# Optimization experiments

Hardware: AMD Instinct MI355X
Metric: run time of the kernel (lower is better)

Reference implementation:

```python
import jax, jax.numpy as jnp
import numpy as np

GROUPS = 32
EPS = 1e-5
NUM_HEADS = 8
HEAD_DIM = 64
CHANNELS = 512


def group_norm(x, scale, bias):
    # x: [b, h, w, c]; normalize over (h, w, channels-within-group)
    b, h, w, c = x.shape
    xg = x.reshape(b, h, w, GROUPS, c // GROUPS)
    mean = jnp.mean(xg, axis=(1, 2, 4), keepdims=True)
    var = jnp.var(xg, axis=(1, 2, 4), keepdims=True)
    xg = (xg - mean) * jax.lax.rsqrt(var + EPS)
    return xg.reshape(b, h, w, c) * scale + bias


def setup_inputs() -> dict:
    key = jax.random.key(0)
    ks = jax.random.split(key, 8)
    b, hs, ws, c = 8, 32, 32, CHANNELS
    inner = NUM_HEADS * HEAD_DIM
    return {
        "x": jax.random.normal(ks[0], (b, hs, ws, c), dtype=jnp.float32),
        "t": jax.random.normal(ks[1], (b,), dtype=jnp.float32),
        "gn_scale": jnp.ones((c,), dtype=jnp.float32),
        "gn_bias": jnp.zeros((c,), dtype=jnp.float32),
        "w_qkv": jax.random.normal(ks[2], (c, 3 * inner), dtype=jnp.float32) * 0.02,
        "b_qkv": jnp.zeros((3 * inner,), dtype=jnp.float32),
        "w_out": jax.random.normal(ks[3], (inner, c), dtype=jnp.float32) * 0.02,
        "b_out": jnp.zeros((c,), dtype=jnp.float32),
    }


def reference(x, t, gn_scale, gn_bias, w_qkv, b_qkv, w_out, b_out):
    b, hs, ws, c = x.shape
    # NOTE: original reassigns x = GroupNorm(x); the residual uses the NORMALIZED x.
    xn = group_norm(x, gn_scale, gn_bias)
    x_flat = xn.reshape(b, hs * ws, c)                      # [b, s, c]
    qkv = x_flat @ w_qkv + b_qkv                            # [b, s, 3*nh*hd]
    qkv = qkv.reshape(b, hs * ws, NUM_HEADS, 3 * HEAD_DIM)
    q, k, v = jnp.split(qkv, 3, axis=-1)                    # each [b, s, nh, hd]
    q = q / jnp.sqrt(jnp.float32(HEAD_DIM))
    q = q.transpose(0, 2, 1, 3)                             # [b, nh, s, hd]
    k = k.transpose(0, 2, 1, 3)
    v = v.transpose(0, 2, 1, 3)
    attn = jax.nn.softmax(jnp.einsum('bhqd,bhkd->bhqk', q, k), axis=-1)
    out = jnp.einsum('bhqk,bhkd->bhqd', attn, v)            # [b, nh, s, hd]
    out = out.transpose(0, 2, 1, 3).reshape(b, hs * ws, NUM_HEADS * HEAD_DIM)
    h = out @ w_out + b_out                                 # [b, s, c]
    h = h.reshape(b, hs, ws, c)
    return xn + h
```

## Files before the change

### kernel.cpp

```cpp
#include <hip/hip_runtime.h>
#include <hip/hip_bf16.h>


#define B_    8
#define S_    1024
#define C_    512
#define NH    8
#define HD    64
#define QKVC  1536
#define GROUPS 32
#define GSIZE  16
#define EPSV   1e-5f
#define QSCL  0.18033688f

using frag8 = __attribute__((ext_vector_type(8))) short;
using f32x4 = __attribute__((ext_vector_type(4))) float;

__device__ __forceinline__ float bf2f(unsigned short u) {
    union { unsigned int i; float f; } v; v.i = ((unsigned int)u) << 16; return v.f;
}
__device__ __forceinline__ unsigned short f2bf(float f) {
    union { float f; unsigned int i; } v; v.f = f;
    unsigned int x = v.i;
    return (unsigned short)((x + 0x7fffu + ((x >> 16) & 1u)) >> 16);
}
__device__ __forceinline__ unsigned int pk2bf(float a, float b) {
    union { float f; unsigned int u; } x, y; x.f = a; y.f = b;
    return __builtin_amdgcn_perm(y.u + 0x8000u, x.u + 0x8000u, 0x07060302u);
}
__device__ __forceinline__ float fexp2(float x) {
#if __has_builtin(__builtin_amdgcn_exp2f)
    return __builtin_amdgcn_exp2f(x);
#else
    return exp2f(x);
#endif
}
__device__ __forceinline__ f32x4 zero4() {
    f32x4 z; z[0] = 0.f; z[1] = 0.f; z[2] = 0.f; z[3] = 0.f; return z;
}
__device__ __forceinline__ void gl_lds(const unsigned short* gp, unsigned short* lp) {
    __builtin_amdgcn_global_load_lds(
        (const __attribute__((address_space(1))) void*)gp,
        (__attribute__((address_space(3))) void*)lp, 16, 0, 0);
}

__global__ __launch_bounds__(256) void prep_kernel(
        const float* __restrict__ w_qkv, const float* __restrict__ w_out,
        unsigned short* __restrict__ wqkvT, unsigned short* __restrict__ woutT,
        const float* __restrict__ x,
        const float* __restrict__ scale, const float* __restrict__ bias,
        unsigned short* __restrict__ xn) {
    __shared__ unsigned short xcache[16384];
    __shared__ float s_red[8];
    int id = blockIdx.x;
    int t = threadIdx.x;
    if (id < 1024) {
        float* tile = (float*)xcache;
        const float* in; unsigned short* out; int N, n0, k0;
        if (id < 768) { in = w_qkv; out = wqkvT; N = QKVC; n0 = (id % 48) * 32; k0 = (id / 48) * 32; }
        else { int i2 = id - 768; in = w_out; out = woutT; N = C_; n0 = (i2 % 16) * 32; k0 = (i2 / 16) * 32; }
        for (int i = 0; i < 4; ++i) {
            int idx = t + i * 256; int r = idx >> 5, c = idx & 31;
            tile[r * 33 + c] = in[(size_t)(k0 + r) * N + n0 + c];
        }
        __syncthreads();
        for (int i = 0; i < 4; ++i) {
            int idx = t + i * 256; int r = idx >> 5, c = idx & 31;
            out[(size_t)(n0 + r) * C_ + k0 + c] = f2bf(tile[c * 33 + r]);
        }
        return;
    }
    int bg = id - 1024;
    int b = bg >> 5, g = bg & 31;
    const float* xb = x + (size_t)b * S_ * C_;

    float sum = 0.f, ss = 0.f;
    for (int i = 0; i < 16; ++i) {
        int idx = t + i * 256;
        int row = idx >> 2, j = idx & 3;
        float4 v = *(const float4*)(xb + (size_t)row * C_ + g * GSIZE + j * 4);
        sum += v.x + v.y + v.z + v.w;
        ss  += v.x * v.x + v.y * v.y + v.z * v.z + v.w * v.w;
        uint2 c;
        c.x = pk2bf(v.x, v.y);
        c.y = pk2bf(v.z, v.w);
        *(uint2*)(&xcache[idx * 4]) = c;
    }
    for (int off = 1; off < 64; off <<= 1) {
        sum += __shfl_xor(sum, off);
        ss  += __shfl_xor(ss,  off);
    }
    int wid = t >> 6;
    if ((t & 63) == 0) { s_red[wid] = sum; s_red[4 + wid] = ss; }
    __syncthreads();
    sum = s_red[0] + s_red[1] + s_red[2] + s_red[3];
    ss  = s_red[4] + s_red[5] + s_red[6] + s_red[7];
    float mean = sum * (1.f / 16384.f);
    float var  = ss * (1.f / 16384.f) - mean * mean;
    float rinv = rsqrtf(var + EPSV);

    float sc[16], bi[16];
    for (int u = 0; u < 16; ++u) {
        sc[u] = scale[g * GSIZE + u];
        bi[u] = bias[g * GSIZE + u];
    }
    for (int i = 0; i < 16; ++i) {
        int idx = t + i * 256;
        int row = idx >> 2, j = idx & 3;
        uint2 c = *(const uint2*)(&xcache[idx * 4]);
        float v0 = bf2f((unsigned short)(c.x & 0xffffu));
        float v1 = bf2f((unsigned short)(c.x >> 16));
        float v2 = bf2f((unsigned short)(c.y & 0xffffu));
        float v3 = bf2f((unsigned short)(c.y >> 16));
        int c0 = j * 4;
        float f0 = (v0 - mean) * rinv * sc[c0 + 0] + bi[c0 + 0];
        float f1 = (v1 - mean) * rinv * sc[c0 + 1] + bi[c0 + 1];
        float f2 = (v2 - mean) * rinv * sc[c0 + 2] + bi[c0 + 2];
        float f3 = (v3 - mean) * rinv * sc[c0 + 3] + bi[c0 + 3];
        uint2 o;
        o.x = pk2bf(f0, f1);
        o.y = pk2bf(f2, f3);
        *(uint2*)(xn + (size_t)b * S_ * C_ + (size_t)row * C_ + g * GSIZE + c0) = o;
    }
}

__global__ __launch_bounds__(256) void gemm_qkv_kernel(
        const unsigned short* __restrict__ A,
        const unsigned short* __restrict__ Bt,
        const float* __restrict__ bias,
        unsigned short* __restrict__ outA,
        unsigned short* __restrict__ outV) {
    __shared__ unsigned short As[2][128 * 32];
    __shared__ unsigned short Bs[2][128 * 32];
    unsigned int flat = blockIdx.y * 12u + blockIdx.x;
    unsigned int nid = (flat & 7u) * 96u + (flat >> 3);
    int my = nid / 12u, mx = nid % 12u;
    int m0 = my * 128, n0 = mx * 128;
    int t = threadIdx.x;
    int wid = t >> 6, lane = t & 63;
    int quad = lane >> 4, l16 = lane & 15;
    int wm = (wid >> 1) * 64, wn = (wid & 1) * 64;

    f32x4 acc[4][4];
    for (int mi = 0; mi < 4; ++mi)
        for (int ni = 0; ni < 4; ++ni) acc[mi][ni] = zero4();

    int srow = t >> 2, sseg = t & 3;
    auto stage = [&](int k0, int buf) {
        for (int i = 0; i < 2; ++i) {
            gl_lds(A + (size_t)(m0 + i * 64 + srow) * C_ + k0 + sseg * 8,
                   &As[buf][(size_t)(i * 256 + wid * 64) * 8]);
            gl_lds(Bt + (size_t)(n0 + i * 64 + srow) * C_ + k0 + sseg * 8,
                   &Bs[buf][(size_t)(i * 256 + wid * 64) * 8]);
        }
    };

    stage(0, 0);
    const int nk = C_ >> 5;
    for (int i = 0; i < nk; ++i) {
        __syncthreads();
        if (i + 1 < nk) stage((i + 1) << 5, (i + 1) & 1);
        int buf = i & 1;

        frag8 bfrag[4], afrag[4];
        for (int ni = 0; ni < 4; ++ni)
            bfrag[ni] = *(const frag8*)(&Bs[buf][(wn + ni * 16 + l16) * 32 + quad * 8]);
        for (int mi = 0; mi < 4; ++mi)
            afrag[mi] = *(const frag8*)(&As[buf][(wm + mi * 16 + l16) * 32 + quad * 8]);

        for (int mi = 0; mi < 4; ++mi)
            for (int ni = 0; ni < 4; ++ni)
                acc[mi][ni] = __builtin_amdgcn_mfma_f32_16x16x32_bf16(
                    afrag[mi], bfrag[ni], acc[mi][ni], 0, 0, 0);
    }

    for (int ni = 0; ni < 4; ++ni) {
        int c0 = n0 + wn + ni * 16;
        float bv = bias[c0 + l16];
        int h = c0 / 192, rr = c0 % 192;
        if (rr >= 128) {
            int d = rr - 128 + l16;
            int bidx = m0 >> 10;
            unsigned short* vp = outV + (((size_t)bidx * NH + h) * HD + d) * S_
                               + (m0 & 1023) + wm + quad * 4;
            for (int mi = 0; mi < 4; ++mi) {
                uint2 pk;
                pk.x = pk2bf(acc[mi][ni][0] + bv, acc[mi][ni][1] + bv);
                pk.y = pk2bf(acc[mi][ni][2] + bv, acc[mi][ni][3] + bv);
                *(uint2*)(vp + mi * 16) = pk;
            }
        } else {
            float scl = (rr < 64) ? QSCL : 1.0f;
            int colk = h * 128 + rr + l16;
            for (int mi = 0; mi < 4; ++mi)
                for (int r = 0; r < 4; ++r) {
                    int row = m0 + wm + mi * 16 + quad * 4 + r;
                    outA[(size_t)row * 1024 + colk] = f2bf((acc[mi][ni][r] + bv) * scl);
                }
        }
    }
}

__global__ __launch_bounds__(256) void gemm_out_kernel(
        const unsigned short* __restrict__ A,
        const unsigned short* __restrict__ Bt,
        const float* __restrict__ bias,
        const unsigned short* __restrict__ resid,
        float* __restrict__ outF) {
    __shared__ unsigned short As[2][64 * 32];
    __shared__ unsigned short Bs[2][128 * 32];
    unsigned int flat = blockIdx.x;
    unsigned int nid = (flat & 7u) * 64u + (flat >> 3);
    int my = nid >> 2, mx = nid & 3;
    int m0 = my * 64, n0 = mx * 128;
    int t = threadIdx.x;
    int wid = t >> 6, lane = t & 63;
    int quad = lane >> 4, l16 = lane & 15;
    int wm = (wid >> 1) * 32, wn = (wid & 1) * 64;

    f32x4 acc[2][4];
    for (int mi = 0; mi < 2; ++mi)
        for (int ni = 0; ni < 4; ++ni) acc[mi][ni] = zero4();

    int srow = t >> 2, sseg = t & 3;
    auto stage = [&](int k0, int buf) {
        gl_lds(A + (size_t)(m0 + srow) * C_ + k0 + sseg * 8,
               &As[buf][(size_t)wid * 512]);
        for (int i = 0; i < 2; ++i)
            gl_lds(Bt + (size_t)(n0 + i * 64 + srow) * C_ + k0 + sseg * 8,
                   &Bs[buf][(size_t)(i * 256 + wid * 64) * 8]);
    };

    stage(0, 0);
    const int nk = C_ >> 5;
    for (int i = 0; i < nk; ++i) {
        __syncthreads();
        if (i + 1 < nk) stage((i + 1) << 5, (i + 1) & 1);
        int buf = i & 1;

        frag8 bfrag[4], afrag[2];
        for (int ni = 0; ni < 4; ++ni)
            bfrag[ni] = *(const frag8*)(&Bs[buf][(wn + ni * 16 + l16) * 32 + quad * 8]);
        for (int mi = 0; mi < 2; ++mi)
            afrag[mi] = *(const frag8*)(&As[buf][(wm + mi * 16 + l16) * 32 + quad * 8]);

        for (int mi = 0; mi < 2; ++mi)
            for (int ni = 0; ni < 4; ++ni)
                acc[mi][ni] = __builtin_amdgcn_mfma_f32_16x16x32_bf16(
                    afrag[mi], bfrag[ni], acc[mi][ni], 0, 0, 0);
    }

    for (int ni = 0; ni < 4; ++ni) {
        int col = n0 + wn + ni * 16 + l16;
        float bv = bias[col];
        for (int mi = 0; mi < 2; ++mi)
            for (int r = 0; r < 4; ++r) {
                int row = m0 + wm + mi * 16 + quad * 4 + r;
                float v = acc[mi][ni][r] + bv + bf2f(resid[(size_t)row * C_ + col]);
                outF[(size_t)row * C_ + col] = v;
            }
    }
}

__global__ __launch_bounds__(256) void attn_kernel(
        const unsigned short* __restrict__ kq,
        const unsigned short* __restrict__ vT,
        unsigned short* __restrict__ attn_out) {
    int i = blockIdx.x;
    int xcd = i & 7, slot = i >> 3;
    int bh = xcd * 8 + (slot >> 3);
    int qt = slot & 7;
    int b = bh >> 3, h = bh & 7;

    int t = threadIdx.x;
    int wid = t >> 6, lane = t & 63, quad = lane >> 4, l16 = lane & 15;
    int q0 = qt * 128 + wid * 32;

    __shared__ unsigned short Ks[2][2][2048];
    __shared__ unsigned short Vs[2][2][2048];

    const unsigned short* qrow0 = kq + ((size_t)b * S_ + q0 + l16) * 1024 + h * 128;
    const unsigned short* qrow1 = qrow0 + (size_t)16 * 1024;
    frag8 qf[2][2];
    qf[0][0] = *(const frag8*)(qrow0 + quad * 8);
    qf[0][1] = *(const frag8*)(qrow0 + 32 + quad * 8);
    qf[1][0] = *(const frag8*)(qrow1 + quad * 8);
    qf[1][1] = *(const frag8*)(qrow1 + 32 + quad * 8);

    frag8 ones;
    for (int i2 = 0; i2 < 8; ++i2) ones[i2] = (short)0x3f80;

    f32x4 o[2][4], ol[2];
    for (int g = 0; g < 2; ++g) {
        ol[g] = zero4();
        for (int dt = 0; dt < 4; ++dt) o[g][dt] = zero4();
    }

    const unsigned short* kbase = kq + (size_t)b * S_ * 1024 + h * 128 + 64;
    const unsigned short* vbase = vT + ((size_t)b * NH + h) * HD * S_;

    int kdh = wid & 1, krh = wid >> 1;
    int krow = krh * 16 + (lane >> 2);
    int kseg = (lane & 3) ^ ((lane >> 3) & 3);
    int vd = wid * 16 + (lane >> 2);
    int vseg = lane & 3;
    int vkh = vseg >> 1, vsp = vseg & 1;
    int vsw = (lane >> 3) & 3;
    int vo1 = (((vsp * 2) ^ vsw) * 8) + vkh * 4;
    int vo2 = (((vsp * 2 + 1) ^ vsw) * 8) + vkh * 4;

    int ksw = (l16 >> 1) & 3;

    auto stageK = [&](int j0, int buf, int half) {
        gl_lds(kbase + (size_t)(j0 + krow) * 1024 + kdh * 32 + kseg * 8,
               &Ks[buf][half][kdh * 1024 + krh * 512]);
    };
    auto loadV = [&](int j0) {
        return *(const uint4*)(vbase + (size_t)vd * S_ + j0 + vseg * 8);
    };
    auto writeV = [&](uint4 w, int buf, int half) {
        unsigned short* vdst = &Vs[buf][half][vd * 32];
        uint2 g1; g1.x = w.x; g1.y = w.y;
        uint2 g2; g2.x = w.z; g2.y = w.w;
        *(uint2*)(vdst + vo1) = g1;
        *(uint2*)(vdst + vo2) = g2;
    };

    stageK(0, 0, 0);  stageK(32, 0, 1);
    writeV(loadV(0), 0, 0);  writeV(loadV(32), 0, 1);

    for (int it = 0; it < S_ / 64; ++it) {
        int cur = it & 1, nxt = cur ^ 1;
        __syncthreads();
        uint4 vn0, vn1;
        bool more = (it < S_ / 64 - 1);
        if (more) {
            int jn = (it + 1) * 64;
            stageK(jn, nxt, 0);
            stageK(jn + 32, nxt, 1);
            vn0 = loadV(jn);
            vn1 = loadV(jn + 32);
        }

        for (int half = 0; half < 2; ++half) {
            frag8 kf[2][2];
            for (int kh = 0; kh < 2; ++kh)
                for (int dh = 0; dh < 2; ++dh)
                    kf[kh][dh] = *(const frag8*)(&Ks[cur][half][dh * 1024
                        + (kh * 16 + l16) * 32 + ((quad ^ ksw) * 8)]);

            frag8 vf[4];
            for (int dt = 0; dt < 4; ++dt)
                vf[dt] = *(const frag8*)(&Vs[cur][half][(dt * 16 + l16) * 32
                        + ((quad ^ ksw) * 8)]);

            for (int g = 0; g < 2; ++g) {
                f32x4 s0 = zero4(), s1 = zero4();
                __builtin_amdgcn_s_setprio(1);
                s0 = __builtin_amdgcn_mfma_f32_16x16x32_bf16(kf[0][0], qf[g][0], s0, 0, 0, 0);
                s0 = __builtin_amdgcn_mfma_f32_16x16x32_bf16(kf[0][1], qf[g][1], s0, 0, 0, 0);
                s1 = __builtin_amdgcn_mfma_f32_16x16x32_bf16(kf[1][0], qf[g][0], s1, 0, 0, 0);
                s1 = __builtin_amdgcn_mfma_f32_16x16x32_bf16(kf[1][1], qf[g][1], s1, 0, 0, 0);
                __builtin_amdgcn_s_setprio(0);

                union { frag8 f; unsigned int u[4]; } pfu;
                pfu.u[0] = pk2bf(fexp2(s0[0]), fexp2(s0[1]));
                pfu.u[1] = pk2bf(fexp2(s0[2]), fexp2(s0[3]));
                pfu.u[2] = pk2bf(fexp2(s1[0]), fexp2(s1[1]));
                pfu.u[3] = pk2bf(fexp2(s1[2]), fexp2(s1[3]));

                __builtin_amdgcn_s_setprio(1);
                ol[g] = __builtin_amdgcn_mfma_f32_16x16x32_bf16(pfu.f, ones, ol[g], 0, 0, 0);
                for (int dt = 0; dt < 4; ++dt)
                    o[g][dt] = __builtin_amdgcn_mfma_f32_16x16x32_bf16(pfu.f, vf[dt], o[g][dt], 0, 0, 0);
                __builtin_amdgcn_s_setprio(0);
            }
        }

        if (more) {
            writeV(vn0, nxt, 0);
            writeV(vn1, nxt, 1);
        }
    }

    for (int g = 0; g < 2; ++g)
        for (int r = 0; r < 4; ++r) {
            float inv = 1.0f / ol[g][r];
            int qrw = q0 + g * 16 + quad * 4 + r;
            for (int dt = 0; dt < 4; ++dt) {
                int ch = h * HD + dt * 16 + l16;
                attn_out[((size_t)b * S_ + qrw) * C_ + ch] = f2bf(o[g][dt][r] * inv);
            }
        }
}

extern "C" void kernel_launch(void* const* d_in, const int* in_sizes, int n_in,
                              void* d_out, int out_size, void* d_ws, size_t ws_size,
                              hipStream_t stream) {
    const float* x        = (const float*)d_in[0];
    const float* gn_scale = (const float*)d_in[2];
    const float* gn_bias  = (const float*)d_in[3];
    const float* w_qkv    = (const float*)d_in[4];
    const float* b_qkv    = (const float*)d_in[5];
    const float* w_out    = (const float*)d_in[6];
    const float* b_out    = (const float*)d_in[7];
    float* out = (float*)d_out;

    char* ws = (char*)d_ws;
    unsigned short* xn    = (unsigned short*)(ws);
    unsigned short* kq    = (unsigned short*)(ws + ((size_t)8  << 20));
    unsigned short* attn  = (unsigned short*)(ws + ((size_t)24 << 20));
    unsigned short* vT    = (unsigned short*)(ws + ((size_t)32 << 20));
    unsigned short* wqkvT = (unsigned short*)(ws + ((size_t)40 << 20));
    unsigned short* woutT = (unsigned short*)(ws + ((size_t)40 << 20) + ((size_t)3 << 19));

    prep_kernel<<<dim3(1280), 256, 0, stream>>>(
        w_qkv, w_out, wqkvT, woutT, x, gn_scale, gn_bias, xn);

    gemm_qkv_kernel<<<dim3(QKVC / 128, (B_ * S_) / 128), 256, 0, stream>>>(
        xn, wqkvT, b_qkv, kq, vT);

    attn_kernel<<<dim3(512), 256, 0, stream>>>(kq, vT, attn);

    gemm_out_kernel<<<dim3(512), 256, 0, stream>>>(
        attn, woutT, b_out, xn, out);
}
```

Measured before the change: 152.3 us.

## Swizzle LDS tiles in GEMMs, remap groupnorm blocks per XCD, pack transpose stores

Result: no change. 149.9 us (-1.5%).

```diff
diff --git a/kernel.cpp b/kernel.cpp
--- a/kernel.cpp
+++ b/kernel.cpp
@@ -64,14 +64,18 @@
             tile[r * 33 + c] = in[(size_t)(k0 + r) * N + n0 + c];
         }
         __syncthreads();
-        for (int i = 0; i < 4; ++i) {
-            int idx = t + i * 256; int r = idx >> 5, c = idx & 31;
-            out[(size_t)(n0 + r) * C_ + k0 + c] = f2bf(tile[c * 33 + r]);
+        for (int i = 0; i < 2; ++i) {
+            int idx = t + i * 256;
+            int r = idx >> 4, c2 = (idx & 15) * 2;
+            unsigned int pk = pk2bf(tile[c2 * 33 + r], tile[(c2 + 1) * 33 + r]);
+            *(unsigned int*)(&out[(size_t)(n0 + r) * C_ + k0 + c2]) = pk;
         }
         return;
     }
-    int bg = id - 1024;
-    int b = bg >> 5, g = bg & 31;
+    int s = id - 1024;
+    int xcd = s & 7, u = s >> 3;
+    int gp = xcd * 16 + (u >> 1);
+    int b = gp >> 4, g = ((gp & 15) << 1) | (u & 1);
     const float* xb = x + (size_t)b * S_ * C_;
 
     float sum = 0.f, ss = 0.f;
@@ -100,9 +104,9 @@
     float rinv = rsqrtf(var + EPSV);
 
     float sc[16], bi[16];
-    for (int u = 0; u < 16; ++u) {
-        sc[u] = scale[g * GSIZE + u];
-        bi[u] = bias[g * GSIZE + u];
+    for (int u2 = 0; u2 < 16; ++u2) {
+        sc[u2] = scale[g * GSIZE + u2];
+        bi[u2] = bias[g * GSIZE + u2];
     }
     for (int i = 0; i < 16; ++i) {
         int idx = t + i * 256;
@@ -145,15 +149,18 @@
     for (int mi = 0; mi < 4; ++mi)
         for (int ni = 0; ni < 4; ++ni) acc[mi][ni] = zero4();
 
-    int srow = t >> 2, sseg = t & 3;
+    int srow = t >> 2;
+    int sseg_sw = (t & 3) ^ ((t >> 3) & 3);
     auto stage = [&](int k0, int buf) {
         for (int i = 0; i < 2; ++i) {
-            gl_lds(A + (size_t)(m0 + i * 64 + srow) * C_ + k0 + sseg * 8,
+            gl_lds(A + (size_t)(m0 + i * 64 + srow) * C_ + k0 + sseg_sw * 8,
                    &As[buf][(size_t)(i * 256 + wid * 64) * 8]);
-            gl_lds(Bt + (size_t)(n0 + i * 64 + srow) * C_ + k0 + sseg * 8,
+            gl_lds(Bt + (size_t)(n0 + i * 64 + srow) * C_ + k0 + sseg_sw * 8,
                    &Bs[buf][(size_t)(i * 256 + wid * 64) * 8]);
         }
     };
+
+    int rsw8 = ((l16 >> 1) & 3) * 8;
 
     stage(0, 0);
     const int nk = C_ >> 5;
@@ -164,9 +171,9 @@
 
         frag8 bfrag[4], afrag[4];
         for (int ni = 0; ni < 4; ++ni)
-            bfrag[ni] = *(const frag8*)(&Bs[buf][(wn + ni * 16 + l16) * 32 + quad * 8]);
+            bfrag[ni] = *(const frag8*)(&Bs[buf][(wn + ni * 16 + l16) * 32 + ((quad * 8) ^ rsw8)]);
         for (int mi = 0; mi < 4; ++mi)
-            afrag[mi] = *(const frag8*)(&As[buf][(wm + mi * 16 + l16) * 32 + quad * 8]);
+            afrag[mi] = *(const frag8*)(&As[buf][(wm + mi * 16 + l16) * 32 + ((quad * 8) ^ rsw8)]);
 
         for (int mi = 0; mi < 4; ++mi)
             for (int ni = 0; ni < 4; ++ni)
@@ -222,14 +229,17 @@
     for (int mi = 0; mi < 2; ++mi)
         for (int ni = 0; ni < 4; ++ni) acc[mi][ni] = zero4();
 
-    int srow = t >> 2, sseg = t & 3;
+    int srow = t >> 2;
+    int sseg_sw = (t & 3) ^ ((t >> 3) & 3);
     auto stage = [&](int k0, int buf) {
-        gl_lds(A + (size_t)(m0 + srow) * C_ + k0 + sseg * 8,
+        gl_lds(A + (size_t)(m0 + srow) * C_ + k0 + sseg_sw * 8,
                &As[buf][(size_t)wid * 512]);
         for (int i = 0; i < 2; ++i)
-            gl_lds(Bt + (size_t)(n0 + i * 64 + srow) * C_ + k0 + sseg * 8,
+            gl_lds(Bt + (size_t)(n0 + i * 64 + srow) * C_ + k0 + sseg_sw * 8,
                    &Bs[buf][(size_t)(i * 256 + wid * 64) * 8]);
     };
+
+    int rsw8 = ((l16 >> 1) & 3) * 8;
 
     stage(0, 0);
     const int nk = C_ >> 5;
@@ -240,9 +250,9 @@
 
         frag8 bfrag[4], afrag[2];
         for (int ni = 0; ni < 4; ++ni)
-            bfrag[ni] = *(const frag8*)(&Bs[buf][(wn + ni * 16 + l16) * 32 + quad * 8]);
+            bfrag[ni] = *(const frag8*)(&Bs[buf][(wn + ni * 16 + l16) * 32 + ((quad * 8) ^ rsw8)]);
         for (int mi = 0; mi < 2; ++mi)
-            afrag[mi] = *(const frag8*)(&As[buf][(wm + mi * 16 + l16) * 32 + quad * 8]);
+            afrag[mi] = *(const frag8*)(&As[buf][(wm + mi * 16 + l16) * 32 + ((quad * 8) ^ rsw8)]);
 
         for (int mi = 0; mi < 2; ++mi)
             for (int ni = 0; ni < 4; ++ni)
```
